# Optimization experiments

Measured on AMD Instinct MI355X. Metric: run time of the kernel, lower is better.

## Reference

```python
import jax, jax.numpy as jnp
import numpy as np

NI, ND, NH = 64, 64, 4
NB, NLOC, NNEI = 4, 2048, 64


def setup_inputs() -> dict:
    key = jax.random.key(0)
    ks = jax.random.split(key, 7)
    g1 = jax.random.normal(ks[0], (NB, NLOC, NI), dtype=jnp.float32)
    gg1 = jax.random.normal(ks[1], (NB, NLOC, NNEI, NI), dtype=jnp.float32)
    nlist_mask = jax.random.randint(ks[2], (NB, NLOC, NNEI), 0, 2).astype(bool)
    # torch Linear weight (out, in); store transposed for x @ W
    Wq = jax.random.normal(ks[3], (NI, ND * NH), dtype=jnp.float32) * (1.0 / np.sqrt(NI))
    Wkv = jax.random.normal(ks[4], (NI, (ND + NI) * NH), dtype=jnp.float32) * (1.0 / np.sqrt(NI))
    Wh = jax.random.normal(ks[5], (NI * NH, NI), dtype=jnp.float32) * (1.0 / np.sqrt(NI * NH))
    bh = jax.random.normal(ks[6], (NI,), dtype=jnp.float32) * 0.01
    return {"g1": g1, "gg1": gg1, "nlist_mask": nlist_mask,
            "Wq": Wq, "Wkv": Wkv, "Wh": Wh, "bh": bh}


def reference(g1, gg1, nlist_mask, Wq, Wkv, Wh, bh):
    nb, nloc, nnei = nlist_mask.shape
    ni, nd, nh = NI, ND, NH
    # q: (nb, nloc, nh, nd)
    q = (g1 @ Wq).reshape(nb, nloc, nd, nh).transpose(0, 1, 3, 2)
    # kv: (nb, nloc, nnei, nd, 2*nh) -> (nb, nloc, 2*nh, nnei, nd); valid since ni == nd
    kv = (gg1 @ Wkv).reshape(nb, nloc, nnei, nd, 2 * nh).transpose(0, 1, 4, 2, 3)
    k = kv[:, :, :nh]          # (nb, nloc, nh, nnei, nd)
    v = kv[:, :, nh:2 * nh]    # (nb, nloc, nh, nnei, nd)
    attnw = jnp.einsum('blhd,blhjd->blhj', q, k) / np.sqrt(nd).astype(np.float32)
    m = nlist_mask[:, :, None, :]  # (nb, nloc, 1, nnei)
    attnw = jnp.where(m, attnw, -jnp.inf)
    attnw = jax.nn.softmax(attnw, axis=-1)
    attnw = jnp.where(m, attnw, 0.0)
    ret = jnp.einsum('blhj,blhjd->blhd', attnw, v).reshape(nb, nloc, nh * ni)
    return ret @ Wh + bh
```

## Files before the change

### kernel.cpp

```cpp
#include <hip/hip_runtime.h>
#include <hip/hip_fp16.h>
#include <math.h>

#define NATOM 8192

namespace {

typedef _Float16 half8 __attribute__((ext_vector_type(8)));
typedef _Float16 half2t __attribute__((ext_vector_type(2)));
typedef float f32x4 __attribute__((ext_vector_type(4)));

__global__ void pack_weights(const float* __restrict__ Wkv,
                             const float* __restrict__ Wq,
                             const float* __restrict__ Wh,
                             _Float16* __restrict__ out) {
  int tid = blockIdx.x * 256 + threadIdx.x;
  if (tid < 32768) {
    int i = tid >> 9, c = tid & 511;
    int ks = i >> 5, jj = i & 7, lqk = (i >> 3) & 3;
    int d = c >> 3, e = c & 7, isv = e >> 2, h = e & 3;
    int T = isv * 16 + (d >> 2);
    int m = ((d & 3) << 2) | h;
    int l = lqk * 16 + m;
    out[(((T * 2 + ks) * 64) + l) * 8 + jj] = (_Float16)Wkv[i * 512 + c];
  } else if (tid < 49152) {
    int idx = tid - 32768;
    int i = idx >> 8, c = idx & 255;
    out[32768 + c * 64 + i] = (_Float16)Wq[i * 256 + c];
  } else {
    int idx = tid - 49152;
    int k = idx >> 6, c = idx & 63;
    out[49152 + c * 256 + k] = (_Float16)Wh[k * 64 + c];
  }
}

__device__ __forceinline__ float dot8(half8 a, half8 b, float acc) {
  acc = __builtin_amdgcn_fdot2((half2t){a[0], a[1]}, (half2t){b[0], b[1]}, acc, false);
  acc = __builtin_amdgcn_fdot2((half2t){a[2], a[3]}, (half2t){b[2], b[3]}, acc, false);
  acc = __builtin_amdgcn_fdot2((half2t){a[4], a[5]}, (half2t){b[4], b[5]}, acc, false);
  acc = __builtin_amdgcn_fdot2((half2t){a[6], a[7]}, (half2t){b[6], b[7]}, acc, false);
  return acc;
}

__global__ __launch_bounds__(256, 2)
void local_atten_kernel(const float* __restrict__ g1,
                        const float* __restrict__ gg1,
                        const int* __restrict__ mask,
                        const _Float16* __restrict__ wpack,
                        const float* __restrict__ bh,
                        float* __restrict__ out) {
  __shared__ __align__(16) __half gs[4][4096];
  __shared__ __align__(16) float  qs[4][256];
  __shared__ __align__(16) __half rets[4][256];
  __shared__ __align__(16) __half g1s[4][64];

  const _Float16* wkvp = wpack;
  const _Float16* wqp  = wpack + 32768;
  const _Float16* whp  = wpack + 49152;

  const int t = threadIdx.x;
  const int lane = t & 63;
  const int wave = t >> 6;
  const int lq = lane >> 4;
  const int lr = lane & 15;
  const int atom = blockIdx.x * 4 + wave;

  __half* gsw  = gs[wave];
  float*  qsw  = qs[wave];
  __half* retw = rets[wave];
  __half* g1w  = g1s[wave];

  int mreg[4];
#pragma unroll
  for (int jt = 0; jt < 4; ++jt)
    mreg[jt] = mask[(size_t)atom * 64 + jt * 16 + lr];

  const half8* ap_base = reinterpret_cast<const half8*>(wkvp);
  half8 a0 = ap_base[lane];
  half8 a1 = ap_base[64 + lane];

  g1w[lane] = __float2half(g1[(size_t)atom * 64 + lane]);

  {
    const float4* src = reinterpret_cast<const float4*>(gg1 + (size_t)atom * 4096);
#pragma unroll
    for (int bat = 0; bat < 2; ++bat) {
      float4 v[8];
#pragma unroll
      for (int r = 0; r < 8; ++r) v[r] = src[lane + 64 * (bat * 8 + r)];
#pragma unroll
      for (int r = 0; r < 8; ++r) {
        int idx4 = lane + 64 * (bat * 8 + r);
        int j = idx4 >> 4;
        int i4 = (idx4 & 15) << 2;
        __half2 h01 = __floats2half2_rn(v[r].x, v[r].y);
        __half2 h23 = __floats2half2_rn(v[r].z, v[r].w);
        int g = i4 >> 3;
        int addr = j * 64 + ((g ^ (j & 7)) << 3) + (i4 & 7);
        union { __half2 h[2]; uint2 u; } pk;
        pk.h[0] = h01; pk.h[1] = h23;
        *reinterpret_cast<uint2*>(&gsw[addr]) = pk.u;
      }
    }
  }

  {
    const half8* grow = reinterpret_cast<const half8*>(g1w);
    float4 qv;
#pragma unroll
    for (int cc = 0; cc < 4; ++cc) {
      const half8* wrow = reinterpret_cast<const half8*>(wqp + (lane * 4 + cc) * 64);
      float qacc = 0.f;
#pragma unroll
      for (int ks = 0; ks < 8; ++ks) qacc = dot8(wrow[ks], grow[ks], qacc);
      qv[cc] = qacc;
    }
    *reinterpret_cast<float4*>(&qsw[lane * 4]) = qv;
  }

  half8 bfrag[4][2];
  {
    const __half* bp0 = &gsw[lr * 64 + ((lq ^ (lr & 7)) << 3)];
    const __half* bp1 = &gsw[lr * 64 + (((4 + lq) ^ (lr & 7)) << 3)];
#pragma unroll
    for (int jt = 0; jt < 4; ++jt) {
      bfrag[jt][0] = *reinterpret_cast<const half8*>(bp0 + jt * 1024);
      bfrag[jt][1] = *reinterpret_cast<const half8*>(bp1 + jt * 1024);
    }
  }

  float sacc[4][4];
#pragma unroll
  for (int jt = 0; jt < 4; ++jt)
#pragma unroll
    for (int h = 0; h < 4; ++h) sacc[jt][h] = 0.f;

#pragma unroll
  for (int T = 0; T < 16; ++T) {
    half8 na0 = ap_base[(T + 1) * 128 + lane];
    half8 na1 = ap_base[(T + 1) * 128 + 64 + lane];
    const int d = T * 4 + lq;
    float4 q4 = *reinterpret_cast<const float4*>(&qsw[d * 4]);
#pragma unroll
    for (int jt = 0; jt < 4; ++jt) {
      f32x4 acc = {0.f, 0.f, 0.f, 0.f};
      acc = __builtin_amdgcn_mfma_f32_16x16x32_f16(a0, bfrag[jt][0], acc, 0, 0, 0);
      acc = __builtin_amdgcn_mfma_f32_16x16x32_f16(a1, bfrag[jt][1], acc, 0, 0, 0);
      sacc[jt][0] = fmaf(acc[0], q4.x, sacc[jt][0]);
      sacc[jt][1] = fmaf(acc[1], q4.y, sacc[jt][1]);
      sacc[jt][2] = fmaf(acc[2], q4.z, sacc[jt][2]);
      sacc[jt][3] = fmaf(acc[3], q4.w, sacc[jt][3]);
    }
    a0 = na0; a1 = na1;
  }

#pragma unroll
  for (int jt = 0; jt < 4; ++jt)
#pragma unroll
    for (int h = 0; h < 4; ++h) {
      sacc[jt][h] += __shfl_xor(sacc[jt][h], 16);
      sacc[jt][h] += __shfl_xor(sacc[jt][h], 32);
    }

  float aw[4][4];
  {
#pragma unroll
    for (int jt = 0; jt < 4; ++jt)
#pragma unroll
      for (int h = 0; h < 4; ++h)
        sacc[jt][h] = mreg[jt] ? sacc[jt][h] * 0.125f : -INFINITY;
#pragma unroll
    for (int h = 0; h < 4; ++h) {
      float mx = fmaxf(fmaxf(sacc[0][h], sacc[1][h]), fmaxf(sacc[2][h], sacc[3][h]));
#pragma unroll
      for (int off = 8; off > 0; off >>= 1) mx = fmaxf(mx, __shfl_xor(mx, off));
      float p0 = mreg[0] ? __expf(sacc[0][h] - mx) : 0.f;
      float p1 = mreg[1] ? __expf(sacc[1][h] - mx) : 0.f;
      float p2 = mreg[2] ? __expf(sacc[2][h] - mx) : 0.f;
      float p3 = mreg[3] ? __expf(sacc[3][h] - mx) : 0.f;
      float sum = p0 + p1 + p2 + p3;
#pragma unroll
      for (int off = 8; off > 0; off >>= 1) sum += __shfl_xor(sum, off);
      float inv = (sum > 0.f) ? (1.f / sum) : 0.f;
      aw[0][h] = p0 * inv; aw[1][h] = p1 * inv;
      aw[2][h] = p2 * inv; aw[3][h] = p3 * inv;
    }
  }

#pragma unroll
  for (int Ti = 0; Ti < 16; ++Ti) {
    const int T = 16 + Ti;
    half8 na0 = a0, na1 = a1;
    if (Ti < 15) {
      na0 = ap_base[(T + 1) * 128 + lane];
      na1 = ap_base[(T + 1) * 128 + 64 + lane];
    }
    float part[4] = {0.f, 0.f, 0.f, 0.f};
#pragma unroll
    for (int jt = 0; jt < 4; ++jt) {
      f32x4 acc = {0.f, 0.f, 0.f, 0.f};
      acc = __builtin_amdgcn_mfma_f32_16x16x32_f16(a0, bfrag[jt][0], acc, 0, 0, 0);
      acc = __builtin_amdgcn_mfma_f32_16x16x32_f16(a1, bfrag[jt][1], acc, 0, 0, 0);
      part[0] = fmaf(acc[0], aw[jt][0], part[0]);
      part[1] = fmaf(acc[1], aw[jt][1], part[1]);
      part[2] = fmaf(acc[2], aw[jt][2], part[2]);
      part[3] = fmaf(acc[3], aw[jt][3], part[3]);
    }
#pragma unroll
    for (int r = 0; r < 4; ++r) {
      part[r] += __shfl_xor(part[r], 1);
      part[r] += __shfl_xor(part[r], 2);
      part[r] += __shfl_xor(part[r], 4);
      part[r] += __shfl_xor(part[r], 8);
    }
    if (lr == 0) {
      const int d = Ti * 4 + lq;
#pragma unroll
      for (int r = 0; r < 4; ++r) retw[r * 64 + d] = __float2half(part[r]);
    }
    a0 = na0; a1 = na1;
  }

  {
    const half8* wrow = reinterpret_cast<const half8*>(whp + lane * 256);
    const half8* rrow = reinterpret_cast<const half8*>(retw);
    float o0 = 0.f, o1 = 0.f;
#pragma unroll
    for (int ks = 0; ks < 16; ++ks) {
      o0 = dot8(wrow[ks], rrow[ks], o0);
      o1 = dot8(wrow[16 + ks], rrow[16 + ks], o1);
    }
    out[(size_t)atom * 64 + lane] = o0 + o1 + bh[lane];
  }
}

}

extern "C" void kernel_launch(void* const* d_in, const int* in_sizes, int n_in,
                              void* d_out, int out_size, void* d_ws, size_t ws_size,
                              hipStream_t stream) {
  const float* g1   = (const float*)d_in[0];
  const float* gg1  = (const float*)d_in[1];
  const int*   mask = (const int*)d_in[2];
  const float* Wq   = (const float*)d_in[3];
  const float* Wkv  = (const float*)d_in[4];
  const float* Wh   = (const float*)d_in[5];
  const float* bh   = (const float*)d_in[6];
  float* out = (float*)d_out;
  (void)in_sizes; (void)n_in; (void)ws_size; (void)out_size;

  _Float16* wpack = (_Float16*)d_ws;
  pack_weights<<<256, 256, 0, stream>>>(Wkv, Wq, Wh, wpack);
  local_atten_kernel<<<NATOM / 4, 256, 0, stream>>>(g1, gg1, mask, wpack, bh, out);
}
```

Measured before the change: 280.4 us.

## Fold Wq·Wk and Wv·Wh into precomputed matrices, attend over raw neighbors

Reassociates the attention algebra. Per-head Wq·Wk^T and Wv·Wh products are precomputed in the weight-pack kernel, so the main kernel projects only g1 to a per-head query in input space. It then scores raw gg1 neighbors with MFMA and computes attention-weighted sums of raw gg1 before applying the fused Wv·Wh. This removes the large per-neighbor K/V projection (32 MFMA tiles per atom per phase), shrinks LDS, and raises the occupancy hint to 4. In exchange it reads gg1 twice from global memory, once transposed with strided scalar loads, and relies on lgkmcnt waits instead of barriers within each wave.

Result: faster. 272.1 us (-3.0%).

```diff
diff --git a/kernel.cpp b/kernel.cpp
--- a/kernel.cpp
+++ b/kernel.cpp
@@ -10,27 +10,34 @@
 typedef _Float16 half2t __attribute__((ext_vector_type(2)));
 typedef float f32x4 __attribute__((ext_vector_type(4)));
 
-__global__ void pack_weights(const float* __restrict__ Wkv,
-                             const float* __restrict__ Wq,
+#define LDS_FENCE()                                        \
+  do {                                                     \
+    asm volatile("s_waitcnt lgkmcnt(0)" ::: "memory");     \
+    __builtin_amdgcn_sched_barrier(0);                     \
+  } while (0)
+
+__global__ void pack_weights(const float* __restrict__ Wq,
+                             const float* __restrict__ Wkv,
                              const float* __restrict__ Wh,
                              _Float16* __restrict__ out) {
   int tid = blockIdx.x * 256 + threadIdx.x;
-  if (tid < 32768) {
-    int i = tid >> 9, c = tid & 511;
-    int ks = i >> 5, jj = i & 7, lqk = (i >> 3) & 3;
-    int d = c >> 3, e = c & 7, isv = e >> 2, h = e & 3;
-    int T = isv * 16 + (d >> 2);
-    int m = ((d & 3) << 2) | h;
-    int l = lqk * 16 + m;
-    out[(((T * 2 + ks) * 64) + l) * 8 + jj] = (_Float16)Wkv[i * 512 + c];
-  } else if (tid < 49152) {
-    int idx = tid - 32768;
-    int i = idx >> 8, c = idx & 255;
-    out[32768 + c * 64 + i] = (_Float16)Wq[i * 256 + c];
+  if (tid < 16384) {
+    int r = tid >> 6, ip = tid & 63;
+    int h = r >> 6, i = r & 63;
+    float acc = 0.f;
+#pragma unroll 8
+    for (int d = 0; d < 64; ++d)
+      acc += Wq[ip * 256 + d * 4 + h] * Wkv[i * 512 + d * 8 + h];
+    out[tid] = (_Float16)acc;
   } else {
-    int idx = tid - 49152;
-    int k = idx >> 6, c = idx & 63;
-    out[49152 + c * 256 + k] = (_Float16)Wh[k * 64 + c];
+    int idx = tid - 16384;
+    int c = idx >> 8, k2 = idx & 255;
+    int h = k2 >> 6, i = k2 & 63;
+    float acc = 0.f;
+#pragma unroll 8
+    for (int d = 0; d < 64; ++d)
+      acc += Wkv[i * 512 + d * 8 + 4 + h] * Wh[(h * 64 + d) * 64 + c];
+    out[16384 + idx] = (_Float16)acc;
   }
 }
 
@@ -42,21 +49,24 @@
   return acc;
 }
 
-__global__ __launch_bounds__(256, 2)
+__device__ __forceinline__ half8 cvt8(float4 a, float4 b) {
+  half8 r;
+  r[0] = (_Float16)a.x; r[1] = (_Float16)a.y; r[2] = (_Float16)a.z; r[3] = (_Float16)a.w;
+  r[4] = (_Float16)b.x; r[5] = (_Float16)b.y; r[6] = (_Float16)b.z; r[7] = (_Float16)b.w;
+  return r;
+}
+
+__global__ __launch_bounds__(256, 4)
 void local_atten_kernel(const float* __restrict__ g1,
                         const float* __restrict__ gg1,
                         const int* __restrict__ mask,
                         const _Float16* __restrict__ wpack,
                         const float* __restrict__ bh,
                         float* __restrict__ out) {
-  __shared__ __align__(16) __half gs[4][4096];
-  __shared__ __align__(16) float  qs[4][256];
-  __shared__ __align__(16) __half rets[4][256];
-  __shared__ __align__(16) __half g1s[4][64];
-
-  const _Float16* wkvp = wpack;
-  const _Float16* wqp  = wpack + 32768;
-  const _Float16* whp  = wpack + 49152;
+  __shared__ __align__(16) _Float16 qa[4][1536];
+
+  const _Float16* Mt  = wpack;
+  const _Float16* Wvh = wpack + 16384;
 
   const int t = threadIdx.x;
   const int lane = t & 63;
@@ -65,170 +75,151 @@
   const int lr = lane & 15;
   const int atom = blockIdx.x * 4 + wave;
 
-  __half* gsw  = gs[wave];
-  float*  qsw  = qs[wave];
-  __half* retw = rets[wave];
-  __half* g1w  = g1s[wave];
+  _Float16* qaw = qa[wave];
+  const float* gbase = gg1 + (size_t)atom * 4096;
 
   int mreg[4];
 #pragma unroll
   for (int jt = 0; jt < 4; ++jt)
     mreg[jt] = mask[(size_t)atom * 64 + jt * 16 + lr];
 
-  const half8* ap_base = reinterpret_cast<const half8*>(wkvp);
-  half8 a0 = ap_base[lane];
-  half8 a1 = ap_base[64 + lane];
-
-  g1w[lane] = __float2half(g1[(size_t)atom * 64 + lane]);
-
+  qaw[1152 + lane] = (_Float16)g1[(size_t)atom * 64 + lane];
+
+#pragma unroll
+  for (int r = 4; r < 16; ++r) qaw[r * 72 + lane] = (_Float16)0.f;
+
+  float4 cur[4];
   {
-    const float4* src = reinterpret_cast<const float4*>(gg1 + (size_t)atom * 4096);
-#pragma unroll
-    for (int bat = 0; bat < 2; ++bat) {
-      float4 v[8];
-#pragma unroll
-      for (int r = 0; r < 8; ++r) v[r] = src[lane + 64 * (bat * 8 + r)];
-#pragma unroll
-      for (int r = 0; r < 8; ++r) {
-        int idx4 = lane + 64 * (bat * 8 + r);
-        int j = idx4 >> 4;
-        int i4 = (idx4 & 15) << 2;
-        __half2 h01 = __floats2half2_rn(v[r].x, v[r].y);
-        __half2 h23 = __floats2half2_rn(v[r].z, v[r].w);
-        int g = i4 >> 3;
-        int addr = j * 64 + ((g ^ (j & 7)) << 3) + (i4 & 7);
-        union { __half2 h[2]; uint2 u; } pk;
-        pk.h[0] = h01; pk.h[1] = h23;
-        *reinterpret_cast<uint2*>(&gsw[addr]) = pk.u;
+    const float4* p = reinterpret_cast<const float4*>(gbase + lr * 64 + lq * 8);
+    cur[0] = p[0]; cur[1] = p[1]; cur[2] = p[8]; cur[3] = p[9];
+  }
+
+  LDS_FENCE();
+
+  {
+    const half8* grow = reinterpret_cast<const half8*>(qaw + 1152);
+    half8 gr[8];
+#pragma unroll
+    for (int ks = 0; ks < 8; ++ks) gr[ks] = grow[ks];
+#pragma unroll
+    for (int h = 0; h < 4; ++h) {
+      const half8* mrow = reinterpret_cast<const half8*>(Mt + (h * 64 + lane) * 64);
+      float a = 0.f;
+#pragma unroll
+      for (int ks = 0; ks < 8; ++ks) a = dot8(mrow[ks], gr[ks], a);
+      qaw[h * 72 + lane] = (_Float16)a;
+    }
+  }
+
+  LDS_FENCE();
+
+  half8 A0 = *reinterpret_cast<const half8*>(qaw + lr * 72 + lq * 8);
+  half8 A1 = *reinterpret_cast<const half8*>(qaw + lr * 72 + 32 + lq * 8);
+
+  f32x4 sa[4];
+#pragma unroll
+  for (int jt = 0; jt < 4; ++jt) {
+    float4 nxt[4];
+    if (jt < 3) {
+      const float4* p =
+          reinterpret_cast<const float4*>(gbase + ((jt + 1) * 16 + lr) * 64 + lq * 8);
+      nxt[0] = p[0]; nxt[1] = p[1]; nxt[2] = p[8]; nxt[3] = p[9];
+    }
+    half8 b0 = cvt8(cur[0], cur[1]);
+    half8 b1 = cvt8(cur[2], cur[3]);
+    f32x4 acc = {0.f, 0.f, 0.f, 0.f};
+    acc = __builtin_amdgcn_mfma_f32_16x16x32_f16(A0, b0, acc, 0, 0, 0);
+    acc = __builtin_amdgcn_mfma_f32_16x16x32_f16(A1, b1, acc, 0, 0, 0);
+    sa[jt] = acc;
+    if (jt < 3) { cur[0] = nxt[0]; cur[1] = nxt[1]; cur[2] = nxt[2]; cur[3] = nxt[3]; }
+  }
+
+  float fT[16];
+#pragma unroll
+  for (int ks = 0; ks < 2; ++ks) {
+    const float* gks = gbase + (ks * 32 + lq * 8) * 64 + lr;
+#pragma unroll
+    for (int e = 0; e < 8; ++e) fT[ks * 8 + e] = gks[e * 64];
+  }
+
+  float awv[4][4];
+#pragma unroll
+  for (int r = 0; r < 4; ++r) {
+    float x[4];
+#pragma unroll
+    for (int jt = 0; jt < 4; ++jt)
+      x[jt] = mreg[jt] ? sa[jt][r] * 0.125f : -INFINITY;
+    float mx = fmaxf(fmaxf(x[0], x[1]), fmaxf(x[2], x[3]));
+#pragma unroll
+    for (int off = 8; off > 0; off >>= 1) mx = fmaxf(mx, __shfl_xor(mx, off));
+    float p[4], sum = 0.f;
+#pragma unroll
+    for (int jt = 0; jt < 4; ++jt) {
+      p[jt] = mreg[jt] ? __expf(x[jt] - mx) : 0.f;
+      sum += p[jt];
+    }
+#pragma unroll
+    for (int off = 8; off > 0; off >>= 1) sum += __shfl_xor(sum, off);
+    float inv = (sum > 0.f) ? (1.f / sum) : 0.f;
+#pragma unroll
+    for (int jt = 0; jt < 4; ++jt) awv[r][jt] = p[jt] * inv;
+  }
+  if (lq == 0) {
+#pragma unroll
+    for (int r = 0; r < 4; ++r)
+#pragma unroll
+      for (int jt = 0; jt < 4; ++jt)
+        qaw[r * 72 + jt * 16 + lr] = (_Float16)awv[r][jt];
+  }
+
+  LDS_FENCE();
+
+  half8 Au0 = *reinterpret_cast<const half8*>(qaw + lr * 72 + lq * 8);
+  half8 Au1 = *reinterpret_cast<const half8*>(qaw + lr * 72 + 32 + lq * 8);
+
+  f32x4 ua[4];
+#pragma unroll
+  for (int it = 0; it < 4; ++it) {
+    float fN[16];
+    if (it < 3) {
+#pragma unroll
+      for (int ks = 0; ks < 2; ++ks) {
+        const float* gks = gbase + (ks * 32 + lq * 8) * 64 + (it + 1) * 16 + lr;
+#pragma unroll
+        for (int e = 0; e < 8; ++e) fN[ks * 8 + e] = gks[e * 64];
       }
     }
-  }
+    half8 b0, b1;
+#pragma unroll
+    for (int e = 0; e < 8; ++e) { b0[e] = (_Float16)fT[e]; b1[e] = (_Float16)fT[8 + e]; }
+    f32x4 acc = {0.f, 0.f, 0.f, 0.f};
+    acc = __builtin_amdgcn_mfma_f32_16x16x32_f16(Au0, b0, acc, 0, 0, 0);
+    acc = __builtin_amdgcn_mfma_f32_16x16x32_f16(Au1, b1, acc, 0, 0, 0);
+    ua[it] = acc;
+    if (it < 3) {
+#pragma unroll
+      for (int e = 0; e < 16; ++e) fT[e] = fN[e];
+    }
+  }
+
+  if (lq == 0) {
+#pragma unroll
+    for (int r = 0; r < 4; ++r)
+#pragma unroll
+      for (int it = 0; it < 4; ++it)
+        qaw[1216 + r * 64 + it * 16 + lr] = (_Float16)ua[it][r];
+  }
+
+  LDS_FENCE();
 
   {
-    const half8* grow = reinterpret_cast<const half8*>(g1w);
-    float4 qv;
-#pragma unroll
-    for (int cc = 0; cc < 4; ++cc) {
-      const half8* wrow = reinterpret_cast<const half8*>(wqp + (lane * 4 + cc) * 64);
-      float qacc = 0.f;
-#pragma unroll
-      for (int ks = 0; ks < 8; ++ks) qacc = dot8(wrow[ks], grow[ks], qacc);
-      qv[cc] = qacc;
-    }
-    *reinterpret_cast<float4*>(&qsw[lane * 4]) = qv;
-  }
-
-  half8 bfrag[4][2];
-  {
-    const __half* bp0 = &gsw[lr * 64 + ((lq ^ (lr & 7)) << 3)];
-    const __half* bp1 = &gsw[lr * 64 + (((4 + lq) ^ (lr & 7)) << 3)];
-#pragma unroll
-    for (int jt = 0; jt < 4; ++jt) {
-      bfrag[jt][0] = *reinterpret_cast<const half8*>(bp0 + jt * 1024);
-      bfrag[jt][1] = *reinterpret_cast<const half8*>(bp1 + jt * 1024);
-    }
-  }
-
-  float sacc[4][4];
-#pragma unroll
-  for (int jt = 0; jt < 4; ++jt)
-#pragma unroll
-    for (int h = 0; h < 4; ++h) sacc[jt][h] = 0.f;
-
-#pragma unroll
-  for (int T = 0; T < 16; ++T) {
-    half8 na0 = ap_base[(T + 1) * 128 + lane];
-    half8 na1 = ap_base[(T + 1) * 128 + 64 + lane];
-    const int d = T * 4 + lq;
-    float4 q4 = *reinterpret_cast<const float4*>(&qsw[d * 4]);
-#pragma unroll
-    for (int jt = 0; jt < 4; ++jt) {
-      f32x4 acc = {0.f, 0.f, 0.f, 0.f};
-      acc = __builtin_amdgcn_mfma_f32_16x16x32_f16(a0, bfrag[jt][0], acc, 0, 0, 0);
-      acc = __builtin_amdgcn_mfma_f32_16x16x32_f16(a1, bfrag[jt][1], acc, 0, 0, 0);
-      sacc[jt][0] = fmaf(acc[0], q4.x, sacc[jt][0]);
-      sacc[jt][1] = fmaf(acc[1], q4.y, sacc[jt][1]);
-      sacc[jt][2] = fmaf(acc[2], q4.z, sacc[jt][2]);
-      sacc[jt][3] = fmaf(acc[3], q4.w, sacc[jt][3]);
-    }
-    a0 = na0; a1 = na1;
-  }
-
-#pragma unroll
-  for (int jt = 0; jt < 4; ++jt)
-#pragma unroll
-    for (int h = 0; h < 4; ++h) {
-      sacc[jt][h] += __shfl_xor(sacc[jt][h], 16);
-      sacc[jt][h] += __shfl_xor(sacc[jt][h], 32);
-    }
-
-  float aw[4][4];
-  {
-#pragma unroll
-    for (int jt = 0; jt < 4; ++jt)
-#pragma unroll
-      for (int h = 0; h < 4; ++h)
-        sacc[jt][h] = mreg[jt] ? sacc[jt][h] * 0.125f : -INFINITY;
-#pragma unroll
-    for (int h = 0; h < 4; ++h) {
-      float mx = fmaxf(fmaxf(sacc[0][h], sacc[1][h]), fmaxf(sacc[2][h], sacc[3][h]));
-#pragma unroll
-      for (int off = 8; off > 0; off >>= 1) mx = fmaxf(mx, __shfl_xor(mx, off));
-      float p0 = mreg[0] ? __expf(sacc[0][h] - mx) : 0.f;
-      float p1 = mreg[1] ? __expf(sacc[1][h] - mx) : 0.f;
-      float p2 = mreg[2] ? __expf(sacc[2][h] - mx) : 0.f;
-      float p3 = mreg[3] ? __expf(sacc[3][h] - mx) : 0.f;
-      float sum = p0 + p1 + p2 + p3;
-#pragma unroll
-      for (int off = 8; off > 0; off >>= 1) sum += __shfl_xor(sum, off);
-      float inv = (sum > 0.f) ? (1.f / sum) : 0.f;
-      aw[0][h] = p0 * inv; aw[1][h] = p1 * inv;
-      aw[2][h] = p2 * inv; aw[3][h] = p3 * inv;
-    }
-  }
-
-#pragma unroll
-  for (int Ti = 0; Ti < 16; ++Ti) {
-    const int T = 16 + Ti;
-    half8 na0 = a0, na1 = a1;
-    if (Ti < 15) {
-      na0 = ap_base[(T + 1) * 128 + lane];
-      na1 = ap_base[(T + 1) * 128 + 64 + lane];
-    }
-    float part[4] = {0.f, 0.f, 0.f, 0.f};
-#pragma unroll
-    for (int jt = 0; jt < 4; ++jt) {
-      f32x4 acc = {0.f, 0.f, 0.f, 0.f};
-      acc = __builtin_amdgcn_mfma_f32_16x16x32_f16(a0, bfrag[jt][0], acc, 0, 0, 0);
-      acc = __builtin_amdgcn_mfma_f32_16x16x32_f16(a1, bfrag[jt][1], acc, 0, 0, 0);
-      part[0] = fmaf(acc[0], aw[jt][0], part[0]);
-      part[1] = fmaf(acc[1], aw[jt][1], part[1]);
-      part[2] = fmaf(acc[2], aw[jt][2], part[2]);
-      part[3] = fmaf(acc[3], aw[jt][3], part[3]);
-    }
-#pragma unroll
-    for (int r = 0; r < 4; ++r) {
-      part[r] += __shfl_xor(part[r], 1);
-      part[r] += __shfl_xor(part[r], 2);
-      part[r] += __shfl_xor(part[r], 4);
-      part[r] += __shfl_xor(part[r], 8);
-    }
-    if (lr == 0) {
-      const int d = Ti * 4 + lq;
-#pragma unroll
-      for (int r = 0; r < 4; ++r) retw[r * 64 + d] = __float2half(part[r]);
-    }
-    a0 = na0; a1 = na1;
-  }
-
-  {
-    const half8* wrow = reinterpret_cast<const half8*>(whp + lane * 256);
-    const half8* rrow = reinterpret_cast<const half8*>(retw);
+    const half8* usp  = reinterpret_cast<const half8*>(qaw + 1216);
+    const half8* wrow = reinterpret_cast<const half8*>(Wvh + lane * 256);
     float o0 = 0.f, o1 = 0.f;
 #pragma unroll
     for (int ks = 0; ks < 16; ++ks) {
-      o0 = dot8(wrow[ks], rrow[ks], o0);
-      o1 = dot8(wrow[16 + ks], rrow[16 + ks], o1);
+      o0 = dot8(wrow[ks], usp[ks], o0);
+      o1 = dot8(wrow[16 + ks], usp[16 + ks], o1);
     }
     out[(size_t)atom * 64 + lane] = o0 + o1 + bh[lane];
   }
@@ -250,6 +241,6 @@
   (void)in_sizes; (void)n_in; (void)ws_size; (void)out_size;
 
   _Float16* wpack = (_Float16*)d_ws;
-  pack_weights<<<256, 256, 0, stream>>>(Wkv, Wq, Wh, wpack);
+  pack_weights<<<128, 256, 0, stream>>>(Wq, Wkv, Wh, wpack);
   local_atten_kernel<<<NATOM / 4, 256, 0, stream>>>(g1, gg1, mask, wpack, bh, out);
 }
```
